# Kernel tuning notes

Hardware: AMD Instinct MI355X
Metric: run time of the kernel (lower is better)

The kernel has to match this reference:

```python
import jax, jax.numpy as jnp
import numpy as np

SELF_DIM = 64
OBST_DIM = 32
NUM_LANDMARKS = 8
HID = 128
IN_DIM = SELF_DIM + OBST_DIM  # 96


def setup_inputs() -> dict:
    key = jax.random.key(0)
    ks = jax.random.split(key, 16)
    B = 1024
    obs = jax.random.normal(ks[0], (B, 1, SELF_DIM + 40 + NUM_LANDMARKS * OBST_DIM), dtype=jnp.float32)

    def w(k, shape, fan_in):
        return (jax.random.normal(k, shape, dtype=jnp.float32) / np.sqrt(fan_in)).astype(jnp.float32)

    return {
        "obs": obs,
        "all_neighbor_obs_size": 40,
        "batch_size": B,
        # Hypernet2: Linear(96->128), tanh, Linear(128->96*128), tanh
        "hw1": w(ks[1], (IN_DIM, HID), IN_DIM), "hb1": jnp.zeros((HID,), jnp.float32),
        "hw2": w(ks[2], (HID, IN_DIM * HID), HID), "hb2": jnp.zeros((IN_DIM * HID,), jnp.float32),
        # neighbor_value_mlp: two Linear(128->128) with tanh
        "vw1": w(ks[3], (HID, HID), HID), "vb1": jnp.zeros((HID,), jnp.float32),
        "vw2": w(ks[4], (HID, HID), HID), "vb2": jnp.zeros((HID,), jnp.float32),
        # attention_mlp: Linear(256->128) tanh, Linear(128->128) tanh, Linear(128->1)
        "aw1": w(ks[5], (2 * HID, HID), 2 * HID), "ab1": jnp.zeros((HID,), jnp.float32),
        "aw2": w(ks[6], (HID, HID), HID), "ab2": jnp.zeros((HID,), jnp.float32),
        "aw3": w(ks[7], (HID, 1), HID), "ab3": jnp.zeros((1,), jnp.float32),
    }


def reference(obs, all_neighbor_obs_size, batch_size,
              hw1, hb1, hw2, hb2, vw1, vb1, vw2, vb2,
              aw1, ab1, aw2, ab2, aw3, ab3):
    B = batch_size
    A = obs.shape[1]  # agents per row (1)
    L = NUM_LANDMARKS

    # slice obstacle block and flatten to per-obstacle rows  [B*A*L, OBST_DIM]
    obs_obstacles = obs[:, :, SELF_DIM + all_neighbor_obs_size:].reshape(-1, OBST_DIM)
    # repeat self-obs along dim 1 (torch .repeat(1, L, 1)) -> [B*A*L, SELF_DIM]
    self_rep = jnp.tile(obs[:, :, :SELF_DIM], (1, L, 1)).reshape(-1, SELF_DIM)
    mlp_input = jnp.concatenate([self_rep, obs_obstacles], axis=1)  # [N, 96]
    N = mlp_input.shape[0]

    # Hypernet2 -> per-instance weight [N, 96, HID]
    h = jnp.tanh(mlp_input @ hw1 + hb1)
    w_flat = jnp.tanh(h @ hw2 + hb2)
    obstacle_w = w_flat.reshape(N, IN_DIM, HID)

    # per-instance matvec + tanh  [N, HID]
    emb = jnp.tanh(jnp.einsum('ni,nio->no', mlp_input, obstacle_w))

    # neighbor value MLP
    vals = jnp.tanh(jnp.tanh(emb @ vw1 + vb1) @ vw2 + vb2)

    # mean pooling over landmarks per batch
    emb_mean = emb.reshape(B, -1, HID).mean(axis=1)  # [B, HID]
    # torch mean.repeat(L, 1): tile whole batch block L times (faithful ordering)
    mean_rep = jnp.tile(emb_mean, (L, 1))  # [B*L, HID]

    att_in = jnp.concatenate([emb, mean_rep], axis=1)  # [N, 2*HID]
    a = jnp.tanh(att_in @ aw1 + ab1)
    a = jnp.tanh(a @ aw2 + ab2)
    logits = (a @ aw3 + ab3).reshape(B, -1)  # [B, L]
    att = jax.nn.softmax(logits, axis=1).reshape(-1, 1)  # [N, 1]

    final = (att * vals).reshape(B, -1, HID).sum(axis=1)  # [B, HID]
    return final.reshape(-1, A, HID)
```

## Files before the change

### kernel.cpp

```cpp
#include <hip/hip_runtime.h>

typedef _Float16 f16x8 __attribute__((ext_vector_type(8)));
typedef float f32x4 __attribute__((ext_vector_type(4)));

__device__ __forceinline__ float tanh_fast(float x){
  float e = __builtin_amdgcn_exp2f(x * 2.88539008177793f);
  return 1.f - 2.f * __builtin_amdgcn_rcpf(1.f + e);
}
__device__ __forceinline__ unsigned short f2h(float f){
  return __builtin_bit_cast(unsigned short, (_Float16)f);
}
__device__ __forceinline__ float h2f(unsigned short u){
  return (float)__builtin_bit_cast(_Float16, u);
}
__device__ __forceinline__ f32x4 mfma16(f16x8 a, f16x8 b, f32x4 c){
  return __builtin_amdgcn_mfma_f32_16x16x32_f16(a, b, c, 0, 0, 0);
}

__device__ __forceinline__ f16x8 ldsA(const unsigned short* buf, int rb, int s, int lane){
  return *(const f16x8*)(buf + (rb*16 + (lane&15))*128 + s*32 + ((lane>>4)<<3));
}

__global__ __launch_bounds__(256) void prep_kernel(
    const float* __restrict__ obs, const float* __restrict__ hw1,
    const float* __restrict__ hb1, const float* __restrict__ hw2,
    const float* __restrict__ vw1, const float* __restrict__ vw2,
    const float* __restrict__ aw1, const float* __restrict__ aw2,
    unsigned short* __restrict__ wt2, unsigned short* __restrict__ vw1t,
    unsigned short* __restrict__ vw2t, unsigned short* __restrict__ aw1t,
    unsigned short* __restrict__ aw2t, unsigned short* __restrict__ h16){
  int b = blockIdx.x, t = threadIdx.x;
  if (b < 1616){
    __shared__ float tile[32][33];
    const float* in; unsigned short* out; int R, C, bx, by;
    if (b < 1536)      { in=hw2; out=wt2;  R=128; C=12288; bx=b%384;      by=b/384; }
    else if (b < 1552) { int q=b-1536; in=vw1; out=vw1t; R=128; C=128; bx=q&3; by=q>>2; }
    else if (b < 1568) { int q=b-1552; in=vw2; out=vw2t; R=128; C=128; bx=q&3; by=q>>2; }
    else if (b < 1600) { int q=b-1568; in=aw1; out=aw1t; R=256; C=128; bx=q&3; by=q>>2; }
    else               { int q=b-1600; in=aw2; out=aw2t; R=128; C=128; bx=q&3; by=q>>2; }
    int c0=bx*32, r0=by*32, tx=t&31, ty=t>>5;
    #pragma unroll
    for (int j=ty; j<32; j+=8) tile[j][tx] = in[(size_t)(r0+j)*C + c0 + tx];
    __syncthreads();
    #pragma unroll
    for (int j=ty; j<32; j+=8) out[(size_t)(c0+j)*R + r0 + tx] = f2h(tile[tx][j]);
  } else {
    __shared__ float w_s[96*128];
    __shared__ float x_s[16*96];
    __shared__ float b_s[128];
    int n0 = (b-1616)*16;
    for (int idx=t; idx<96*128; idx+=256) w_s[idx] = hw1[idx];
    if (t < 128) b_s[t] = hb1[t];
    for (int idx=t; idx<16*96; idx+=256){
      int r = idx/96, i = idx - r*96;
      int n = n0 + r; int bb = n>>3, l = n&7;
      x_s[idx] = (i<64) ? obs[bb*360 + i] : obs[bb*360 + 104 + (l<<5) + (i-64)];
    }
    __syncthreads();
    for (int e=t; e<16*128; e+=256){
      int r = e>>7, o = e&127;
      float acc = b_s[o];
      const float* xr = &x_s[r*96];
      #pragma unroll 4
      for (int i=0;i<96;++i) acc = fmaf(xr[i], w_s[i*128+o], acc);
      h16[(size_t)(n0+r)*128 + o] = f2h(tanh_fast(acc));
    }
  }
}

__global__ __launch_bounds__(512, 2) void k2_hyper(const float* __restrict__ obs,
    const unsigned short* __restrict__ h16, const unsigned short* __restrict__ wt2,
    const float* __restrict__ hb2, float* __restrict__ accg){
  __shared__ float x_s[24*128];
  int t = threadIdx.x, lane = t & 63, w = t >> 6;
  int rt = blockIdx.x >> 2, iq = blockIdx.x & 3;
  int R0 = rt*128, ibase = iq*24;
  int wcol = w*16 + (lane&15);
  int kof  = (lane>>4) << 3;
  int rloc = (lane>>4) << 2;

  for (int idx=t; idx<24*128; idx+=512){
    int il = idx>>7, r = idx&127;
    int i = ibase + il;
    int n = R0 + r; int bb = n>>3, l = n&7;
    x_s[idx] = (i<64) ? obs[bb*360 + i] : obs[bb*360 + 104 + (l<<5) + (i-64)];
  }

  f16x8 af[8][4];
  #pragma unroll
  for (int rb=0; rb<8; ++rb)
    #pragma unroll
    for (int s=0; s<4; ++s)
      af[rb][s] = *(const f16x8*)(h16 + (size_t)(R0 + rb*16 + (lane&15))*128 + s*32 + kof);

  __syncthreads();

  float facc[8][4];
  #pragma unroll
  for (int rb=0;rb<8;++rb)
    #pragma unroll
    for (int reg=0;reg<4;++reg) facc[rb][reg] = 0.f;

  const unsigned short* wp = wt2 + (size_t)(ibase*128 + wcol)*128 + kof;
  const float* bp = hb2 + ibase*128 + wcol;

  f16x8 A0,A1,A2,A3, B0,B1,B2,B3;
  float biasA, biasB;

#define K2L(X0,X1,X2,X3,BI) do{                 \
    X0 = *(const f16x8*)(wp);                   \
    X1 = *(const f16x8*)(wp+32);                \
    X2 = *(const f16x8*)(wp+64);                \
    X3 = *(const f16x8*)(wp+96);                \
    BI = *bp;                                   \
    wp += 16384; bp += 128;                     \
  }while(0)

#define K2C(X0,X1,X2,X3,BI,IL) do{                                       \
    _Pragma("unroll")                                                    \
    for (int rb=0; rb<8; rb+=2){                                         \
      f32x4 a0 = {BI,BI,BI,BI}, a1 = {BI,BI,BI,BI};                      \
      a0 = mfma16(af[rb][0], X0, a0); a1 = mfma16(af[rb+1][0], X0, a1);  \
      a0 = mfma16(af[rb][1], X1, a0); a1 = mfma16(af[rb+1][1], X1, a1);  \
      a0 = mfma16(af[rb][2], X2, a0); a1 = mfma16(af[rb+1][2], X2, a1);  \
      a0 = mfma16(af[rb][3], X3, a0); a1 = mfma16(af[rb+1][3], X3, a1);  \
      f32x4 x0 = *(const f32x4*)(x_s + (IL)*128 + rb*16 + rloc);         \
      f32x4 x1 = *(const f32x4*)(x_s + (IL)*128 + (rb+1)*16 + rloc);     \
      _Pragma("unroll")                                                  \
      for (int reg=0; reg<4; ++reg){                                     \
        facc[rb][reg]   = fmaf(x0[reg], tanh_fast(a0[reg]), facc[rb][reg]);   \
        facc[rb+1][reg] = fmaf(x1[reg], tanh_fast(a1[reg]), facc[rb+1][reg]); \
      }                                                                  \
    }                                                                    \
  }while(0)

  K2L(A0,A1,A2,A3,biasA);
  K2L(B0,B1,B2,B3,biasB);
  for (int il=0; il<22; il+=2){
    K2C(A0,A1,A2,A3,biasA,il);
    K2L(A0,A1,A2,A3,biasA);
    K2C(B0,B1,B2,B3,biasB,il+1);
    K2L(B0,B1,B2,B3,biasB);
  }
  K2C(A0,A1,A2,A3,biasA,22);
  K2C(B0,B1,B2,B3,biasB,23);
#undef K2L
#undef K2C

  #pragma unroll
  for (int rb=0; rb<8; ++rb)
    #pragma unroll
    for (int reg=0; reg<4; ++reg)
      atomicAdd(&accg[(size_t)(R0 + rb*16 + rloc + reg)*128 + wcol], facc[rb][reg]);
}

__global__ __launch_bounds__(256) void k3_mean(const float* __restrict__ accg,
    unsigned short* __restrict__ mean16){
  int t = threadIdx.x, B0 = blockIdx.x*4;
  for (int task=t; task<512; task+=256){
    int bl = task>>7, o = task&127;
    float m = 0.f;
    #pragma unroll
    for (int l=0;l<8;++l)
      m += tanh_fast(accg[(size_t)((B0 + bl)*8 + l)*128 + o]);
    mean16[(size_t)(B0 + bl)*128 + o] = f2h(m * 0.125f);
  }
}

template<int KS>
__device__ __forceinline__ void stage(const unsigned short* inA, const unsigned short* inB,
    const unsigned short* wt, const float* bias, unsigned short* outb, int w, int lane){
  #pragma unroll
  for (int obl=0; obl<2; ++obl){
    int col = ((w*2+obl)<<4) + (lane&15);
    f32x4 a0 = {0.f,0.f,0.f,0.f}, a1v = {0.f,0.f,0.f,0.f};
    #pragma unroll
    for (int s=0;s<KS;++s){
      f16x8 bfr = *(const f16x8*)(wt + (size_t)col*(KS*32) + s*32 + ((lane>>4)<<3));
      f16x8 aa0, aa1;
      if (KS==8 && s>=4){ aa0 = ldsA(inB,0,s-4,lane); aa1 = ldsA(inB,1,s-4,lane); }
      else              { aa0 = ldsA(inA,0,s,lane);   aa1 = ldsA(inA,1,s,lane);   }
      a0  = mfma16(aa0, bfr, a0);
      a1v = mfma16(aa1, bfr, a1v);
    }
    float bb = bias[col];
    #pragma unroll
    for (int reg=0;reg<4;++reg){
      int r0 = ((lane>>4)<<2) + reg;
      outb[r0*128 + col]      = f2h(tanh_fast(a0[reg] + bb));
      outb[(16+r0)*128 + col] = f2h(tanh_fast(a1v[reg] + bb));
    }
  }
}

__global__ __launch_bounds__(256) void k4_mlp(
    const float* __restrict__ accg, const unsigned short* __restrict__ mean16,
    const unsigned short* __restrict__ vw1t, const unsigned short* __restrict__ vw2t,
    const unsigned short* __restrict__ aw1t, const unsigned short* __restrict__ aw2t,
    const float* __restrict__ vb1, const float* __restrict__ vb2,
    const float* __restrict__ ab1, const float* __restrict__ ab2,
    const float* __restrict__ aw3, const float* __restrict__ ab3,
    float* __restrict__ outp){
  __shared__ unsigned short bufE[32*128];
  __shared__ unsigned short bufM[32*128];
  __shared__ unsigned short bufA[32*128];
  __shared__ float fin[4*128];
  __shared__ float lp[32*8];
  __shared__ float att_s[32];
  int t = threadIdx.x, lane = t&63, w = t>>6;
  int R0 = blockIdx.x*32;

  for (int idx=t; idx<4096; idx+=256)
    bufE[idx] = f2h(tanh_fast(accg[(size_t)R0*128 + idx]));
  for (int idx=t; idx<512; idx+=256){
    int r = idx>>4, c8 = (idx&15)<<3;
    int n = R0 + r;
    *(uint4*)(bufM + r*128 + c8) = *(const uint4*)(mean16 + (size_t)(n & 1023)*128 + c8);
  }
  for (int idx=t; idx<512; idx+=256) fin[idx] = 0.f;
  __syncthreads();

  stage<8>(bufE, bufM, aw1t, ab1, bufA, w, lane);
  __syncthreads();
  stage<4>(bufA, nullptr, aw2t, ab2, bufM, w, lane);
  __syncthreads();
  {
    int r = t>>3, seg = t&7;
    float p = 0.f;
    const unsigned short* row = bufM + r*128 + seg*16;
    const float* w3 = aw3 + seg*16;
    #pragma unroll
    for (int k=0;k<16;++k) p += h2f(row[k]) * w3[k];
    lp[r*8+seg] = p;
  }
  __syncthreads();
  if (t < 4){
    float lg[8]; float mx = -1e30f;
    for (int l=0;l<8;++l){
      float s = ab3[0];
      #pragma unroll
      for (int sg=0;sg<8;++sg) s += lp[(t*8+l)*8+sg];
      lg[l] = s; mx = fmaxf(mx, s);
    }
    float sum = 0.f;
    for (int l=0;l<8;++l){ lg[l] = __builtin_amdgcn_exp2f((lg[l]-mx)*1.44269504089f); sum += lg[l]; }
    float inv = __builtin_amdgcn_rcpf(sum);
    for (int l=0;l<8;++l) att_s[t*8+l] = lg[l]*inv;
  }
  __syncthreads();
  stage<4>(bufE, nullptr, vw1t, vb1, bufA, w, lane);
  __syncthreads();
  {
    #pragma unroll
    for (int obl=0; obl<2; ++obl){
      int col = ((w*2+obl)<<4) + (lane&15);
      f32x4 a0 = {0.f,0.f,0.f,0.f}, a1v = {0.f,0.f,0.f,0.f};
      #pragma unroll
      for (int s=0;s<4;++s){
        f16x8 bfr = *(const f16x8*)(vw2t + (size_t)col*128 + s*32 + ((lane>>4)<<3));
        a0  = mfma16(ldsA(bufA,0,s,lane), bfr, a0);
        a1v = mfma16(ldsA(bufA,1,s,lane), bfr, a1v);
      }
      float bb = vb2[col];
      #pragma unroll
      for (int reg=0;reg<4;++reg){
        int r0 = ((lane>>4)<<2) + reg;
        float v0 = tanh_fast(a0[reg]+bb);
        float v1 = tanh_fast(a1v[reg]+bb);
        atomicAdd(&fin[((r0)>>3)*128 + col],    att_s[r0]    * v0);
        atomicAdd(&fin[((16+r0)>>3)*128 + col], att_s[16+r0] * v1);
      }
    }
  }
  __syncthreads();
  for (int idx=t; idx<512; idx+=256){
    int b_loc = idx>>7, o = idx&127;
    outp[(size_t)(R0/8 + b_loc)*128 + o] = fin[idx];
  }
}

extern "C" void kernel_launch(void* const* d_in, const int* in_sizes, int n_in,
                              void* d_out, int out_size, void* d_ws, size_t ws_size,
                              hipStream_t stream){
  const float* obs = (const float*)d_in[0];
  const float* hw1 = (const float*)d_in[3];
  const float* hb1 = (const float*)d_in[4];
  const float* hw2 = (const float*)d_in[5];
  const float* hb2 = (const float*)d_in[6];
  const float* vw1 = (const float*)d_in[7];
  const float* vb1 = (const float*)d_in[8];
  const float* vw2 = (const float*)d_in[9];
  const float* vb2 = (const float*)d_in[10];
  const float* aw1 = (const float*)d_in[11];
  const float* ab1 = (const float*)d_in[12];
  const float* aw2 = (const float*)d_in[13];
  const float* ab2 = (const float*)d_in[14];
  const float* aw3 = (const float*)d_in[15];
  const float* ab3 = (const float*)d_in[16];

  char* ws = (char*)d_ws;
  unsigned short* wt2    = (unsigned short*)(ws);
  unsigned short* mean16 = (unsigned short*)(ws);
  unsigned short* h16    = (unsigned short*)(ws + 3145728);
  float*          accg   = (float*)        (ws + 5242880);
  unsigned short* vw1t   = (unsigned short*)(ws + 9437184);
  unsigned short* vw2t   = (unsigned short*)(ws + 9469952);
  unsigned short* aw1t   = (unsigned short*)(ws + 9502720);
  unsigned short* aw2t   = (unsigned short*)(ws + 9568256);
  float* outp = (float*)d_out;

  hipMemsetAsync(accg, 0, 8192*128*sizeof(float), stream);
  prep_kernel<<<2128, 256, 0, stream>>>(obs, hw1, hb1, hw2, vw1, vw2, aw1, aw2,
                                        wt2, vw1t, vw2t, aw1t, aw2t, h16);
  k2_hyper<<<256, 512, 0, stream>>>(obs, h16, wt2, hb2, accg);
  k3_mean<<<256, 256, 0, stream>>>(accg, mean16);
  k4_mlp<<<256, 256, 0, stream>>>(accg, mean16, vw1t, vw2t, aw1t, aw2t,
                                  vb1, vb2, ab1, ab2, aw3, ab3, outp);
}
```

Before: 120.5 us.

## Stage hypernet weight tiles in LDS with async double buffering and swizzle

The k2_hyper kernel used to stream per-wave weight fragments straight from global memory, with each wave covering all 128 rows. Now each 16384-element weight slice is copied into a double-buffered LDS tile via global_load_lds. The prep kernel writes that weight in an XOR-swizzled layout to avoid LDS bank conflicts. Waves are split into a 4x2 row/column grid so fewer A fragments stay in registers and each B tile is reused from LDS across row groups, at the cost of a barrier per iteration and 64KB of LDS per block. The prep kernel's h computation now handles 32 rows per block instead of 16, cutting the grid size.

```diff
diff --git a/kernel.cpp b/kernel.cpp
--- a/kernel.cpp
+++ b/kernel.cpp
@@ -2,6 +2,8 @@
 
 typedef _Float16 f16x8 __attribute__((ext_vector_type(8)));
 typedef float f32x4 __attribute__((ext_vector_type(4)));
+typedef const __attribute__((address_space(1))) void* as1_cvp;
+typedef __attribute__((address_space(3))) void* as3_vp;
 
 __device__ __forceinline__ float tanh_fast(float x){
   float e = __builtin_amdgcn_exp2f(x * 2.88539008177793f);
@@ -32,32 +34,41 @@
   int b = blockIdx.x, t = threadIdx.x;
   if (b < 1616){
     __shared__ float tile[32][33];
-    const float* in; unsigned short* out; int R, C, bx, by;
-    if (b < 1536)      { in=hw2; out=wt2;  R=128; C=12288; bx=b%384;      by=b/384; }
-    else if (b < 1552) { int q=b-1536; in=vw1; out=vw1t; R=128; C=128; bx=q&3; by=q>>2; }
-    else if (b < 1568) { int q=b-1552; in=vw2; out=vw2t; R=128; C=128; bx=q&3; by=q>>2; }
-    else if (b < 1600) { int q=b-1568; in=aw1; out=aw1t; R=256; C=128; bx=q&3; by=q>>2; }
-    else               { int q=b-1600; in=aw2; out=aw2t; R=128; C=128; bx=q&3; by=q>>2; }
+    const float* in; unsigned short* out; int R, C, bx, by; bool swz;
+    if (b < 1536)      { in=hw2; out=wt2;  R=128; C=12288; bx=b%384;      by=b/384; swz=true; }
+    else if (b < 1552) { int q=b-1536; in=vw1; out=vw1t; R=128; C=128; bx=q&3; by=q>>2; swz=false; }
+    else if (b < 1568) { int q=b-1552; in=vw2; out=vw2t; R=128; C=128; bx=q&3; by=q>>2; swz=false; }
+    else if (b < 1600) { int q=b-1568; in=aw1; out=aw1t; R=256; C=128; bx=q&3; by=q>>2; swz=false; }
+    else               { int q=b-1600; in=aw2; out=aw2t; R=128; C=128; bx=q&3; by=q>>2; swz=false; }
     int c0=bx*32, r0=by*32, tx=t&31, ty=t>>5;
     #pragma unroll
     for (int j=ty; j<32; j+=8) tile[j][tx] = in[(size_t)(r0+j)*C + c0 + tx];
     __syncthreads();
-    #pragma unroll
-    for (int j=ty; j<32; j+=8) out[(size_t)(c0+j)*R + r0 + tx] = f2h(tile[tx][j]);
+    if (swz){
+      #pragma unroll
+      for (int j=ty; j<32; j+=8){
+        int col = c0+j, k = r0+tx;
+        int ig = col>>7, colL = col&127;
+        out[(size_t)ig*16384 + colL*128 + (k ^ ((colL&7)<<3))] = f2h(tile[tx][j]);
+      }
+    } else {
+      #pragma unroll
+      for (int j=ty; j<32; j+=8) out[(size_t)(c0+j)*R + r0 + tx] = f2h(tile[tx][j]);
+    }
   } else {
     __shared__ float w_s[96*128];
-    __shared__ float x_s[16*96];
+    __shared__ float x_s[32*96];
     __shared__ float b_s[128];
-    int n0 = (b-1616)*16;
+    int n0 = (b-1616)*32;
     for (int idx=t; idx<96*128; idx+=256) w_s[idx] = hw1[idx];
     if (t < 128) b_s[t] = hb1[t];
-    for (int idx=t; idx<16*96; idx+=256){
+    for (int idx=t; idx<32*96; idx+=256){
       int r = idx/96, i = idx - r*96;
       int n = n0 + r; int bb = n>>3, l = n&7;
       x_s[idx] = (i<64) ? obs[bb*360 + i] : obs[bb*360 + 104 + (l<<5) + (i-64)];
     }
     __syncthreads();
-    for (int e=t; e<16*128; e+=256){
+    for (int e=t; e<32*128; e+=256){
       int r = e>>7, o = e&127;
       float acc = b_s[o];
       const float* xr = &x_s[r*96];
@@ -68,14 +79,25 @@
   }
 }
 
+__device__ __forceinline__ void stage_tile(const unsigned short* gsrc,
+                                           unsigned short* lbuf, int t){
+  const unsigned short* g = gsrc + t*8;
+  unsigned short* l = lbuf + t*8;
+  #pragma unroll
+  for (int p=0;p<4;++p)
+    __builtin_amdgcn_global_load_lds((as1_cvp)(g + p*4096), (as3_vp)(l + p*4096), 16, 0, 0);
+}
+
 __global__ __launch_bounds__(512, 2) void k2_hyper(const float* __restrict__ obs,
     const unsigned short* __restrict__ h16, const unsigned short* __restrict__ wt2,
     const float* __restrict__ hb2, float* __restrict__ accg){
+  __shared__ unsigned short bts[2][16384];
   __shared__ float x_s[24*128];
   int t = threadIdx.x, lane = t & 63, w = t >> 6;
   int rt = blockIdx.x >> 2, iq = blockIdx.x & 3;
   int R0 = rt*128, ibase = iq*24;
-  int wcol = w*16 + (lane&15);
+  int rg = w & 3, cg = w >> 2;
+  int cl   = lane & 15;
   int kof  = (lane>>4) << 3;
   int rloc = (lane>>4) << 2;
 
@@ -86,72 +108,66 @@
     x_s[idx] = (i<64) ? obs[bb*360 + i] : obs[bb*360 + 104 + (l<<5) + (i-64)];
   }
 
-  f16x8 af[8][4];
-  #pragma unroll
-  for (int rb=0; rb<8; ++rb)
+  f16x8 af[2][4];
+  #pragma unroll
+  for (int rb=0; rb<2; ++rb)
     #pragma unroll
     for (int s=0; s<4; ++s)
-      af[rb][s] = *(const f16x8*)(h16 + (size_t)(R0 + rb*16 + (lane&15))*128 + s*32 + kof);
-
-  __syncthreads();
-
-  float facc[8][4];
-  #pragma unroll
-  for (int rb=0;rb<8;++rb)
-    #pragma unroll
-    for (int reg=0;reg<4;++reg) facc[rb][reg] = 0.f;
-
-  const unsigned short* wp = wt2 + (size_t)(ibase*128 + wcol)*128 + kof;
-  const float* bp = hb2 + ibase*128 + wcol;
-
-  f16x8 A0,A1,A2,A3, B0,B1,B2,B3;
-  float biasA, biasB;
-
-#define K2L(X0,X1,X2,X3,BI) do{                 \
-    X0 = *(const f16x8*)(wp);                   \
-    X1 = *(const f16x8*)(wp+32);                \
-    X2 = *(const f16x8*)(wp+64);                \
-    X3 = *(const f16x8*)(wp+96);                \
-    BI = *bp;                                   \
-    wp += 16384; bp += 128;                     \
-  }while(0)
-
-#define K2C(X0,X1,X2,X3,BI,IL) do{                                       \
-    _Pragma("unroll")                                                    \
-    for (int rb=0; rb<8; rb+=2){                                         \
-      f32x4 a0 = {BI,BI,BI,BI}, a1 = {BI,BI,BI,BI};                      \
-      a0 = mfma16(af[rb][0], X0, a0); a1 = mfma16(af[rb+1][0], X0, a1);  \
-      a0 = mfma16(af[rb][1], X1, a0); a1 = mfma16(af[rb+1][1], X1, a1);  \
-      a0 = mfma16(af[rb][2], X2, a0); a1 = mfma16(af[rb+1][2], X2, a1);  \
-      a0 = mfma16(af[rb][3], X3, a0); a1 = mfma16(af[rb+1][3], X3, a1);  \
-      f32x4 x0 = *(const f32x4*)(x_s + (IL)*128 + rb*16 + rloc);         \
-      f32x4 x1 = *(const f32x4*)(x_s + (IL)*128 + (rb+1)*16 + rloc);     \
-      _Pragma("unroll")                                                  \
-      for (int reg=0; reg<4; ++reg){                                     \
-        facc[rb][reg]   = fmaf(x0[reg], tanh_fast(a0[reg]), facc[rb][reg]);   \
-        facc[rb+1][reg] = fmaf(x1[reg], tanh_fast(a1[reg]), facc[rb+1][reg]); \
-      }                                                                  \
-    }                                                                    \
-  }while(0)
-
-  K2L(A0,A1,A2,A3,biasA);
-  K2L(B0,B1,B2,B3,biasB);
-  for (int il=0; il<22; il+=2){
-    K2C(A0,A1,A2,A3,biasA,il);
-    K2L(A0,A1,A2,A3,biasA);
-    K2C(B0,B1,B2,B3,biasB,il+1);
-    K2L(B0,B1,B2,B3,biasB);
-  }
-  K2C(A0,A1,A2,A3,biasA,22);
-  K2C(B0,B1,B2,B3,biasB,23);
-#undef K2L
-#undef K2C
-
-  #pragma unroll
-  for (int rb=0; rb<8; ++rb)
-    #pragma unroll
-    for (int reg=0; reg<4; ++reg)
-      atomicAdd(&accg[(size_t)(R0 + rb*16 + rloc + reg)*128 + wcol], facc[rb][reg]);
+      af[rb][s] = *(const f16x8*)(h16 + (size_t)(R0 + rg*32 + rb*16 + cl)*128 + s*32 + kof);
+
+  stage_tile(wt2 + (size_t)ibase*16384, bts[0], t);
+  __syncthreads();
+
+  float facc[2][4][4];
+  #pragma unroll
+  for (int rb=0;rb<2;++rb)
+    #pragma unroll
+    for (int ch=0;ch<4;++ch)
+      #pragma unroll
+      for (int reg=0;reg<4;++reg) facc[rb][ch][reg] = 0.f;
+
+  for (int it=0; it<24; ++it){
+    const unsigned short* lb = bts[it&1];
+    if (it < 23) stage_tile(wt2 + (size_t)(ibase+it+1)*16384, bts[(it+1)&1], t);
+    const float* bias_p = hb2 + (ibase+it)*128;
+    float xa[4], xb[4];
+    #pragma unroll
+    for (int reg=0;reg<4;++reg){
+      xa[reg] = x_s[it*128 + rg*32 + rloc + reg];
+      xb[reg] = x_s[it*128 + rg*32 + 16 + rloc + reg];
+    }
+    #pragma unroll
+    for (int ch=0; ch<4; ++ch){
+      int colL = cg*64 + ch*16 + cl;
+      int sx = (colL&7)<<3;
+      const unsigned short* bp = lb + colL*128;
+      f16x8 b0 = *(const f16x8*)(bp + ((  0+kof)^sx));
+      f16x8 b1 = *(const f16x8*)(bp + (( 32+kof)^sx));
+      f16x8 b2 = *(const f16x8*)(bp + (( 64+kof)^sx));
+      f16x8 b3 = *(const f16x8*)(bp + (( 96+kof)^sx));
+      float bi = bias_p[colL];
+      f32x4 a0 = {bi,bi,bi,bi}, a1 = {bi,bi,bi,bi};
+      a0 = mfma16(af[0][0], b0, a0); a1 = mfma16(af[1][0], b0, a1);
+      a0 = mfma16(af[0][1], b1, a0); a1 = mfma16(af[1][1], b1, a1);
+      a0 = mfma16(af[0][2], b2, a0); a1 = mfma16(af[1][2], b2, a1);
+      a0 = mfma16(af[0][3], b3, a0); a1 = mfma16(af[1][3], b3, a1);
+      #pragma unroll
+      for (int reg=0;reg<4;++reg){
+        facc[0][ch][reg] = fmaf(xa[reg], tanh_fast(a0[reg]), facc[0][ch][reg]);
+        facc[1][ch][reg] = fmaf(xb[reg], tanh_fast(a1[reg]), facc[1][ch][reg]);
+      }
+    }
+    __syncthreads();
+  }
+
+  #pragma unroll
+  for (int rb=0; rb<2; ++rb)
+    #pragma unroll
+    for (int ch=0; ch<4; ++ch)
+      #pragma unroll
+      for (int reg=0; reg<4; ++reg)
+        atomicAdd(&accg[(size_t)(R0 + rg*32 + rb*16 + rloc + reg)*128 + cg*64 + ch*16 + cl],
+                  facc[rb][ch][reg]);
 }
 
 __global__ __launch_bounds__(256) void k3_mean(const float* __restrict__ accg,
@@ -310,7 +326,7 @@
   float* outp = (float*)d_out;
 
   hipMemsetAsync(accg, 0, 8192*128*sizeof(float), stream);
-  prep_kernel<<<2128, 256, 0, stream>>>(obs, hw1, hb1, hw2, vw1, vw2, aw1, aw2,
+  prep_kernel<<<1872, 256, 0, stream>>>(obs, hw1, hb1, hw2, vw1, vw2, aw1, aw2,
                                         wt2, vw1t, vw2t, aw1t, aw2t, h16);
   k2_hyper<<<256, 512, 0, stream>>>(obs, h16, wt2, hb2, accg);
   k3_mean<<<256, 256, 0, stream>>>(accg, mean16);
```

Result: no change. 121.2 us (+0.6%).
